# Optimization experiments

Measured on AMD Instinct MI355X. Metric: run time of the kernel, lower is better.

## Reference

```python
import jax, jax.numpy as jnp
import numpy as np

TAU = 1.0      # gumbel-softmax temperature
ALPHA = 0.05   # mixprop alpha
GDEP = 1       # mixprop depth

B, C, H, W = 16, 512, 96, 96
N = 64  # n_classes / codebook size


def setup_inputs() -> dict:
    key = jax.random.key(0)
    ks = jax.random.split(key, 8)
    u = jax.random.uniform(ks[3], (B, N, H, W), dtype=jnp.float32, minval=1e-6, maxval=1.0 - 1e-6)
    gumbel_noise = -jnp.log(-jnp.log(u))  # standard Gumbel(0,1)
    return {
        "x": jax.random.normal(ks[0], (B, C, H, W), dtype=jnp.float32),
        "centers": jax.random.normal(ks[1], (N, C), dtype=jnp.float32) * 0.1,
        "A": jax.random.uniform(ks[2], (N, N), dtype=jnp.float32),
        "gumbel_noise": gumbel_noise,
        "W_bc": jax.random.normal(ks[4], (1, C), dtype=jnp.float32) * 0.05,
        "b_bc": jnp.zeros((1,), dtype=jnp.float32),
        "W_gcn": jax.random.normal(ks[5], (C, 2 * C), dtype=jnp.float32) * 0.03,
        "b_gcn": jnp.zeros((C,), dtype=jnp.float32),
    }


def _mixprop_centers(centers, A, W_gcn, b_gcn):
    # mixprop on the codebook: centers [N, C] viewed as x of shape [1, C, N, 1]
    n = A.shape[0]
    adj = A + jnp.eye(n, dtype=A.dtype)
    a = adj / adj.sum(axis=1, keepdims=True)           # row-normalized adjacency
    xg = centers.T[None, :, :, None]                    # [1, C, N, 1]
    h = xg
    outs = [h]
    for _ in range(GDEP):
        h = ALPHA * xg + (1.0 - ALPHA) * jnp.einsum('ncwl,vw->ncvl', h, a)
        outs.append(h)
    ho = jnp.concatenate(outs, axis=1)                  # [1, (GDEP+1)*C, N, 1]
    new_c = jnp.einsum('oc,bcvl->bovl', W_gcn, ho) + b_gcn[None, :, None, None]
    return new_c[0, :, :, 0].T                          # [N, C]


def reference(x, centers, A, gumbel_noise, W_bc, b_bc, W_gcn, b_gcn):
    n = centers.shape[0]
    # inner products of features with codebook centers
    inner_products = jnp.einsum('bchw,nc->bnhw', x, centers)          # [B, N, H, W]
    # gumbel-softmax with hard (straight-through) assignment over dim 1
    y = jax.nn.softmax((inner_products + gumbel_noise) / TAU, axis=1)
    hard = jax.nn.one_hot(jnp.argmax(y, axis=1), n, dtype=y.dtype, axis=1)
    one_hot = hard + y - jax.lax.stop_gradient(y)
    # quantized features via codebook gather
    z_q = jnp.einsum('bnhw,nd->bdhw', one_hot, centers)               # [B, C, H, W]
    # 1x1 conv binary classifier + global average pool
    heatmap = jnp.einsum('oc,bchw->bohw', W_bc, z_q) + b_bc[None, :, None, None]  # [B,1,H,W]
    logits = heatmap.mean(axis=(2, 3)).squeeze()                      # [B]
    # graph diffusion of the codebook
    new_centers = _mixprop_centers(centers, A, W_gcn, b_gcn)          # [N, C]
    normed_ip = jnp.einsum('bchw,nc->bnhw', x, new_centers)           # [B, N, H, W]
    cluster_probs = jax.nn.one_hot(jnp.argmax(normed_ip, axis=1), n, dtype=normed_ip.dtype, axis=1)
    cluster_loss = -(cluster_probs * jax.nn.softmax(normed_ip, axis=1)).sum(axis=1).mean()
    return heatmap, logits, cluster_loss, inner_products
```

## Files before the change

kernel.cpp:

```cpp
#include <hip/hip_runtime.h>
#include <math.h>

#define BATCH   16
#define CDIM    512
#define HWDIM   9216
#define NCLS    64
#define TILE    128
#define NTILES  72
#define NCHUNK  16
#define NBLOCKS (NTILES * BATCH)

#define LOGOFF  147456
#define LOSSOFF 147472
#define IPOFF   147473

#define WS_S    65536
#define WS_PH   65600
#define WS_PC   66752
#define WS_AP   67904

typedef __attribute__((ext_vector_type(8))) short bf16x8;
typedef __attribute__((ext_vector_type(4))) float f32x4;

__device__ __forceinline__ void split3(float v, float& h, float& m, float& l) {
  float hf = __uint_as_float(__float_as_uint(v) & 0xFFFF0000u);
  float r  = v - hf;
  float mf = __uint_as_float(__float_as_uint(r) & 0xFFFF0000u);
  float r2 = r - mf;
  float lf = __uint_as_float(__float_as_uint(r2) & 0xFFFF0000u);
  h = hf; m = mf; l = lf;
}

__device__ __forceinline__ unsigned packbf(float a, float b) {
  return (__float_as_uint(a) >> 16) | (__float_as_uint(b) & 0xFFFF0000u);
}

__global__ __launch_bounds__(256) void prep_kernel(
    const float* __restrict__ centers, const float* __restrict__ Aadj,
    const float* __restrict__ W_bc, const float* __restrict__ b_bc,
    const float* __restrict__ W_gcn, const float* __restrict__ b_gcn,
    float* __restrict__ ws) {
  __shared__ float c_row[CDIM];
  __shared__ float mix_row[CDIM];
  __shared__ float new_row[CDIM];
  __shared__ float a_n[NCLS];
  __shared__ float red[256];
  const int n = blockIdx.x;
  const int tid = threadIdx.x;

  if (tid < NCLS) a_n[tid] = Aadj[n * NCLS + tid] + (tid == n ? 1.0f : 0.0f);
  __syncthreads();
  if (tid == 0) {
    float ssum = 0.f;
    for (int w = 0; w < NCLS; ++w) ssum += a_n[w];
    red[0] = 1.0f / ssum;
  }
  __syncthreads();
  float inv = red[0];
  __syncthreads();
  if (tid < NCLS) a_n[tid] *= inv;
  __syncthreads();

  float p = 0.f;
  for (int c = tid; c < CDIM; c += 256) {
    float v = centers[n * CDIM + c];
    c_row[c] = v;
    float acc = 0.f;
    #pragma unroll 8
    for (int w = 0; w < NCLS; ++w) acc = fmaf(a_n[w], centers[w * CDIM + c], acc);
    mix_row[c] = 0.05f * v + 0.95f * acc;
    p = fmaf(W_bc[c], v, p);
  }
  red[tid] = p;
  __syncthreads();
  for (int st = 128; st > 0; st >>= 1) {
    if (tid < st) red[tid] += red[tid + st];
    __syncthreads();
  }
  if (tid == 0) ws[WS_S + n] = red[0] + b_bc[0];
  __syncthreads();

  for (int o = tid; o < CDIM; o += 256) {
    const float4* wr0 = (const float4*)(W_gcn + (size_t)o * 1024);
    const float4* wr1 = (const float4*)(W_gcn + (size_t)o * 1024 + 512);
    const float4* cr4 = (const float4*)c_row;
    const float4* mr4 = (const float4*)mix_row;
    float a0 = b_gcn[o], a1 = 0.f, a2 = 0.f, a3 = 0.f;
    #pragma unroll 4
    for (int qk = 0; qk < 128; ++qk) {
      float4 wv = wr0[qk], cv = cr4[qk];
      a0 = fmaf(wv.x, cv.x, a0);
      a1 = fmaf(wv.y, cv.y, a1);
      a2 = fmaf(wv.z, cv.z, a2);
      a3 = fmaf(wv.w, cv.w, a3);
    }
    #pragma unroll 4
    for (int qk = 0; qk < 128; ++qk) {
      float4 wv = wr1[qk], mv = mr4[qk];
      a0 = fmaf(wv.x, mv.x, a0);
      a1 = fmaf(wv.y, mv.y, a1);
      a2 = fmaf(wv.z, mv.z, a2);
      a3 = fmaf(wv.w, mv.w, a3);
    }
    new_row[o] = (a0 + a1) + (a2 + a3);
  }
  __syncthreads();

  if (tid < 128) {
    const int rowsel = tid >> 6;
    const int u = tid & 63;
    const int c = u >> 2, q = u & 3;
    const float* rbuf = rowsel ? new_row : c_row;
    const int mb = (rowsel ? 4 : 0) + (n >> 4);
    const int lane = q * 16 + (n & 15);
    float e[8];
    #pragma unroll
    for (int i = 0; i < 8; ++i) e[i] = rbuf[c * 32 + q * 8 + i];
    unsigned dh[4], dm[4], dl[4];
    #pragma unroll
    for (int d = 0; d < 4; ++d) {
      float h0, m0, l0, h1, m1, l1;
      split3(e[2 * d], h0, m0, l0);
      split3(e[2 * d + 1], h1, m1, l1);
      dh[d] = packbf(h0, h1); dm[d] = packbf(m0, m1); dl[d] = packbf(l0, l1);
    }
    float* dst = ws + WS_AP + (size_t)c * 6144 + (size_t)mb * 256 + (size_t)lane * 4;
    *(uint4*)(dst)        = make_uint4(dh[0], dh[1], dh[2], dh[3]);
    *(uint4*)(dst + 2048) = make_uint4(dm[0], dm[1], dm[2], dm[3]);
    *(uint4*)(dst + 4096) = make_uint4(dl[0], dl[1], dl[2], dl[3]);
  }
}

__global__ __launch_bounds__(256, 3) void main_kernel(
    const float* __restrict__ x, const float* __restrict__ gumbel,
    float* __restrict__ ws, float* __restrict__ out) {
  __shared__ char ldsmem[49152];
  __shared__ float s_sh[NCLS];
  char* buf0 = ldsmem;
  char* buf1 = ldsmem + 24576;

  const int tid = threadIdx.x;
  const int w = tid >> 6, l = tid & 63;
  const int tile = blockIdx.x, b = blockIdx.y;
  const int hw0 = tile * TILE;

  if (tid < NCLS) s_sh[tid] = ws[WS_S + tid];

  const float* xb = x + (size_t)b * CDIM * HWDIM;
  const float* pB = xb + (size_t)(w * 8) * HWDIM + hw0 + l;
  const char* ap = (const char*)(ws + WS_AP);
  const int la16 = l * 16;

  f32x4 cip[8], cnp[8];
  #pragma unroll
  for (int i = 0; i < 8; ++i) {
    cip[i] = (f32x4){0.f, 0.f, 0.f, 0.f};
    cnp[i] = (f32x4){0.f, 0.f, 0.f, 0.f};
  }

  float bre[16];
  bf16x8 A0[5], A1[5];

#define LOAD_A(AS, c_) do {                                                   \
    const char* asrc = ap + (size_t)(c_) * 24576;                             \
    AS[0] = *(const bf16x8*)(asrc + w * 1024 + la16);                         \
    AS[1] = *(const bf16x8*)(asrc + 8192 + w * 1024 + la16);                  \
    AS[2] = *(const bf16x8*)(asrc + 16384 + w * 1024 + la16);                 \
    AS[3] = *(const bf16x8*)(asrc + (4 + w) * 1024 + la16);                   \
    AS[4] = *(const bf16x8*)(asrc + 8192 + (4 + w) * 1024 + la16);            \
  } while (0)

#define LOAD_B(c_) do {                                                       \
    const size_t koff = (size_t)(c_) * 32 * HWDIM;                            \
    _Pragma("unroll")                                                         \
    for (int j = 0; j < 8; ++j) {                                             \
      bre[j]     = pB[koff + (size_t)j * HWDIM];                              \
      bre[8 + j] = pB[koff + (size_t)j * HWDIM + 64];                         \
    }                                                                         \
  } while (0)

#define WRITE_B(WB) do {                                                      \
    _Pragma("unroll")                                                         \
    for (int hh = 0; hh < 2; ++hh) {                                          \
      unsigned dh[4], dm[4], dl[4];                                           \
      _Pragma("unroll")                                                       \
      for (int d = 0; d < 4; ++d) {                                           \
        float h0, m0, l0, h1, m1, l1;                                         \
        split3(bre[hh * 8 + 2 * d], h0, m0, l0);                              \
        split3(bre[hh * 8 + 2 * d + 1], h1, m1, l1);                          \
        dh[d] = packbf(h0, h1); dm[d] = packbf(m0, m1); dl[d] = packbf(l0, l1);\
      }                                                                       \
      char* basep = (WB) + ((((l >> 4) + hh * 4) * 64) + (w << 4) + (l & 15)) * 16; \
      *(uint4*)(basep)         = make_uint4(dh[0], dh[1], dh[2], dh[3]);      \
      *(uint4*)(basep + 8192)  = make_uint4(dm[0], dm[1], dm[2], dm[3]);      \
      *(uint4*)(basep + 16384) = make_uint4(dl[0], dl[1], dl[2], dl[3]);      \
    }                                                                         \
  } while (0)

#define CHUNK(c_, RB, WB, AC, AN) do {                                        \
    if ((c_) + 1 < NCHUNK) { LOAD_A(AN, (c_) + 1); LOAD_B((c_) + 1); }        \
    _Pragma("unroll")                                                         \
    for (int nb = 0; nb < 8; ++nb) {                                          \
      bf16x8 bH = *(const bf16x8*)((RB) + nb * 1024 + la16);                  \
      bf16x8 bM = *(const bf16x8*)((RB) + 8192 + nb * 1024 + la16);           \
      bf16x8 bL = *(const bf16x8*)((RB) + 16384 + nb * 1024 + la16);          \
      cip[nb] = __builtin_amdgcn_mfma_f32_16x16x32_bf16(AC[0], bH, cip[nb], 0, 0, 0); \
      cip[nb] = __builtin_amdgcn_mfma_f32_16x16x32_bf16(AC[0], bM, cip[nb], 0, 0, 0); \
      cip[nb] = __builtin_amdgcn_mfma_f32_16x16x32_bf16(AC[1], bH, cip[nb], 0, 0, 0); \
      cip[nb] = __builtin_amdgcn_mfma_f32_16x16x32_bf16(AC[0], bL, cip[nb], 0, 0, 0); \
      cip[nb] = __builtin_amdgcn_mfma_f32_16x16x32_bf16(AC[1], bM, cip[nb], 0, 0, 0); \
      cip[nb] = __builtin_amdgcn_mfma_f32_16x16x32_bf16(AC[2], bH, cip[nb], 0, 0, 0); \
      cnp[nb] = __builtin_amdgcn_mfma_f32_16x16x32_bf16(AC[3], bH, cnp[nb], 0, 0, 0); \
      cnp[nb] = __builtin_amdgcn_mfma_f32_16x16x32_bf16(AC[3], bM, cnp[nb], 0, 0, 0); \
      cnp[nb] = __builtin_amdgcn_mfma_f32_16x16x32_bf16(AC[4], bH, cnp[nb], 0, 0, 0); \
    }                                                                         \
    if ((c_) + 1 < NCHUNK) WRITE_B(WB);                                       \
    __syncthreads();                                                          \
  } while (0)

  LOAD_A(A0, 0);
  LOAD_B(0);
  WRITE_B(buf0);
  __syncthreads();

  #pragma unroll 1
  for (int cc = 0; cc < NCHUNK; cc += 2) {
    CHUNK(cc, buf0, buf1, A0, A1);
    CHUNK(cc + 1, buf1, buf0, A1, A0);
  }

  float* pvv  = (float*)ldsmem;
  int*   pvi  = (int*)(ldsmem + 2048);
  float* pnm  = (float*)(ldsmem + 4096);
  float* pns  = (float*)(ldsmem + 6144);
  float* m2   = (float*)(ldsmem + 8192);
  float* hbuf = (float*)(ldsmem + 8704);
  float* cbuf = (float*)(ldsmem + 9216);

  const size_t bn = (size_t)b * NCLS;
  float* ipo = out + IPOFF;
  const int rbase = 16 * w + ((l >> 4) & 3) * 4;
  const int c15 = l & 15;

  float bv[8]; int bi[8]; float nm[8];
  #pragma unroll
  for (int nb = 0; nb < 8; ++nb) {
    const int hw = hw0 + nb * 16 + c15;
    float best = -1e30f; int besti = 0;
    #pragma unroll
    for (int r = 0; r < 4; ++r) {
      const int n = rbase + r;
      const float v = cip[nb][r];
      ipo[(bn + n) * HWDIM + hw] = v;
      const float t = v + gumbel[(bn + n) * HWDIM + hw];
      if (t > best) { best = t; besti = n; }
    }
    bv[nb] = best; bi[nb] = besti;
    float m = cnp[nb][0];
    m = fmaxf(m, cnp[nb][1]); m = fmaxf(m, cnp[nb][2]); m = fmaxf(m, cnp[nb][3]);
    nm[nb] = m;
  }
  #pragma unroll
  for (int nb = 0; nb < 8; ++nb) {
    #pragma unroll
    for (int mk = 16; mk <= 32; mk <<= 1) {
      float ov = __shfl_xor(bv[nb], mk);
      int   oi = __shfl_xor(bi[nb], mk);
      if (ov > bv[nb] || (ov == bv[nb] && oi < bi[nb])) { bv[nb] = ov; bi[nb] = oi; }
      nm[nb] = fmaxf(nm[nb], __shfl_xor(nm[nb], mk));
    }
  }
  if ((l >> 4) == 0) {
    #pragma unroll
    for (int nb = 0; nb < 8; ++nb) {
      pvv[w * 128 + nb * 16 + l] = bv[nb];
      pvi[w * 128 + nb * 16 + l] = bi[nb];
      pnm[w * 128 + nb * 16 + l] = nm[nb];
    }
  }
  __syncthreads();

  if (tid < 128) {
    float v = pvv[tid]; int i = pvi[tid];
    #pragma unroll
    for (int ww = 1; ww < 4; ++ww) {
      float v2 = pvv[ww * 128 + tid]; int i2 = pvi[ww * 128 + tid];
      if (v2 > v || (v2 == v && i2 < i)) { v = v2; i = i2; }
    }
    float h = s_sh[i];
    hbuf[tid] = h;
    out[(size_t)b * HWDIM + hw0 + tid] = h;
    float m = pnm[tid];
    #pragma unroll
    for (int ww = 1; ww < 4; ++ww) m = fmaxf(m, pnm[ww * 128 + tid]);
    m2[tid] = m;
  }
  __syncthreads();

  #pragma unroll
  for (int nb = 0; nb < 8; ++nb) {
    const float mm = m2[nb * 16 + c15];
    float s = __expf(cnp[nb][0] - mm) + __expf(cnp[nb][1] - mm)
            + __expf(cnp[nb][2] - mm) + __expf(cnp[nb][3] - mm);
    s += __shfl_xor(s, 16);
    s += __shfl_xor(s, 32);
    if ((l >> 4) == 0) pns[w * 128 + nb * 16 + l] = s;
  }
  __syncthreads();

  if (tid < 128) {
    float S = pns[tid] + pns[128 + tid] + pns[256 + tid] + pns[384 + tid];
    cbuf[tid] = 1.0f / S;
  }
  __syncthreads();

  if (tid < 64) {
    float hs = hbuf[tid] + hbuf[tid + 64];
    float cs = cbuf[tid] + cbuf[tid + 64];
    #pragma unroll
    for (int o = 32; o > 0; o >>= 1) {
      hs += __shfl_down(hs, o);
      cs += __shfl_down(cs, o);
    }
    if (tid == 0) {
      ws[WS_PH + b * NTILES + tile] = hs;
      ws[WS_PC + b * NTILES + tile] = cs;
    }
  }
#undef LOAD_A
#undef LOAD_B
#undef WRITE_B
#undef CHUNK
}

__global__ __launch_bounds__(256) void finish_kernel(
    const float* __restrict__ ws, float* __restrict__ out) {
  __shared__ double sred[256];
  const int tid = threadIdx.x;
  {
    int bb = tid >> 4, lane = tid & 15;
    double s = 0.0;
    for (int t = lane; t < NTILES; t += 16) s += (double)ws[WS_PH + bb * NTILES + t];
    #pragma unroll
    for (int o = 8; o > 0; o >>= 1) s += __shfl_down(s, o, 16);
    if (lane == 0) out[LOGOFF + bb] = (float)(s / (double)HWDIM);
  }
  double c = 0.0;
  for (int i = tid; i < BATCH * NTILES; i += 256) c += (double)ws[WS_PC + i];
  sred[tid] = c;
  __syncthreads();
  for (int st = 128; st > 0; st >>= 1) {
    if (tid < st) sred[tid] += sred[tid + st];
    __syncthreads();
  }
  if (tid == 0) out[LOSSOFF] = (float)(-sred[0] / (double)(BATCH * HWDIM));
}

extern "C" void kernel_launch(void* const* d_in, const int* in_sizes, int n_in,
                              void* d_out, int out_size, void* d_ws, size_t ws_size,
                              hipStream_t stream) {
  const float* x       = (const float*)d_in[0];
  const float* centers = (const float*)d_in[1];
  const float* Aadj    = (const float*)d_in[2];
  const float* gumbel  = (const float*)d_in[3];
  const float* W_bc    = (const float*)d_in[4];
  const float* b_bc    = (const float*)d_in[5];
  const float* W_gcn   = (const float*)d_in[6];
  const float* b_gcn   = (const float*)d_in[7];
  float* out = (float*)d_out;
  float* ws  = (float*)d_ws;

  hipLaunchKernelGGL(prep_kernel, dim3(NCLS), dim3(256), 0, stream,
                     centers, Aadj, W_bc, b_bc, W_gcn, b_gcn, ws);
  hipLaunchKernelGGL(main_kernel, dim3(NTILES, BATCH), dim3(256), 0, stream,
                     x, gumbel, ws, out);
  hipLaunchKernelGGL(finish_kernel, dim3(1), dim3(256), 0, stream, ws, out);
}
```

Before: 176.2 us.

## Switch main GEMM to 32x32x16 MFMA with 2x2 wave tiling

Replaces the 16x16x32 bf16 MFMA tiling (each wave owning 16 classes across 8 column blocks) with 32x32x16 MFMA, where waves form a 2x2 grid of 32-class by 64-column tiles. The prep kernel and the LDS B-staging layouts are rearranged to match the new operand fragment layout. The epilogue reductions are rewritten for the 32x32 accumulator layout, needing fewer cross-wave partials. This aims to cut LDS B-fragment reads per MFMA and use the larger MFMA shape, at the cost of doubling the A-fragment registers held per wave.

```diff
diff --git a/kernel.cpp b/kernel.cpp
--- a/kernel.cpp
+++ b/kernel.cpp
@@ -8,7 +8,6 @@
 #define TILE    128
 #define NTILES  72
 #define NCHUNK  16
-#define NBLOCKS (NTILES * BATCH)
 
 #define LOGOFF  147456
 #define LOSSOFF 147472
@@ -20,7 +19,7 @@
 #define WS_AP   67904
 
 typedef __attribute__((ext_vector_type(8))) short bf16x8;
-typedef __attribute__((ext_vector_type(4))) float f32x4;
+typedef __attribute__((ext_vector_type(16))) float f32x16;
 
 __device__ __forceinline__ void split3(float v, float& h, float& m, float& l) {
   float hf = __uint_as_float(__float_as_uint(v) & 0xFFFF0000u);
@@ -109,13 +108,15 @@
   if (tid < 128) {
     const int rowsel = tid >> 6;
     const int u = tid & 63;
-    const int c = u >> 2, q = u & 3;
+    const int c = u >> 2;
+    const int s = (u >> 1) & 1;
+    const int hh = u & 1;
     const float* rbuf = rowsel ? new_row : c_row;
-    const int mb = (rowsel ? 4 : 0) + (n >> 4);
-    const int lane = q * 16 + (n & 15);
+    const int mt = (rowsel ? 2 : 0) + (n >> 5);
+    const int lane = (n & 31) + 32 * hh;
     float e[8];
     #pragma unroll
-    for (int i = 0; i < 8; ++i) e[i] = rbuf[c * 32 + q * 8 + i];
+    for (int i = 0; i < 8; ++i) e[i] = rbuf[c * 32 + s * 16 + hh * 8 + i];
     unsigned dh[4], dm[4], dl[4];
     #pragma unroll
     for (int d = 0; d < 4; ++d) {
@@ -124,7 +125,7 @@
       split3(e[2 * d + 1], h1, m1, l1);
       dh[d] = packbf(h0, h1); dm[d] = packbf(m0, m1); dl[d] = packbf(l0, l1);
     }
-    float* dst = ws + WS_AP + (size_t)c * 6144 + (size_t)mb * 256 + (size_t)lane * 4;
+    float* dst = ws + WS_AP + (size_t)c * 6144 + (size_t)(s * 4 + mt) * 256 + (size_t)lane * 4;
     *(uint4*)(dst)        = make_uint4(dh[0], dh[1], dh[2], dh[3]);
     *(uint4*)(dst + 2048) = make_uint4(dm[0], dm[1], dm[2], dm[3]);
     *(uint4*)(dst + 4096) = make_uint4(dl[0], dl[1], dl[2], dl[3]);
@@ -141,79 +142,94 @@
 
   const int tid = threadIdx.x;
   const int w = tid >> 6, l = tid & 63;
+  const int mh = w & 1, nh = w >> 1;
+  const int h = l >> 5, c31 = l & 31;
   const int tile = blockIdx.x, b = blockIdx.y;
   const int hw0 = tile * TILE;
 
   if (tid < NCLS) s_sh[tid] = ws[WS_S + tid];
 
   const float* xb = x + (size_t)b * CDIM * HWDIM;
-  const float* pB = xb + (size_t)(w * 8) * HWDIM + hw0 + l;
+  const float* pB = xb + (size_t)(h * 8) * HWDIM + hw0 + w * 32 + c31;
   const char* ap = (const char*)(ws + WS_AP);
   const int la16 = l * 16;
 
-  f32x4 cip[8], cnp[8];
+  f32x16 cip[2], cnp[2];
   #pragma unroll
-  for (int i = 0; i < 8; ++i) {
-    cip[i] = (f32x4){0.f, 0.f, 0.f, 0.f};
-    cnp[i] = (f32x4){0.f, 0.f, 0.f, 0.f};
+  for (int i = 0; i < 2; ++i) {
+    cip[i] = (f32x16)(0.f);
+    cnp[i] = (f32x16)(0.f);
   }
 
   float bre[16];
-  bf16x8 A0[5], A1[5];
+  bf16x8 A0[10], A1[10];
 
 #define LOAD_A(AS, c_) do {                                                   \
     const char* asrc = ap + (size_t)(c_) * 24576;                             \
-    AS[0] = *(const bf16x8*)(asrc + w * 1024 + la16);                         \
-    AS[1] = *(const bf16x8*)(asrc + 8192 + w * 1024 + la16);                  \
-    AS[2] = *(const bf16x8*)(asrc + 16384 + w * 1024 + la16);                 \
-    AS[3] = *(const bf16x8*)(asrc + (4 + w) * 1024 + la16);                   \
-    AS[4] = *(const bf16x8*)(asrc + 8192 + (4 + w) * 1024 + la16);            \
+    AS[0] = *(const bf16x8*)(asrc + (0 + mh) * 1024 + la16);                  \
+    AS[1] = *(const bf16x8*)(asrc + 8192 + (0 + mh) * 1024 + la16);           \
+    AS[2] = *(const bf16x8*)(asrc + 16384 + (0 + mh) * 1024 + la16);          \
+    AS[3] = *(const bf16x8*)(asrc + (2 + mh) * 1024 + la16);                  \
+    AS[4] = *(const bf16x8*)(asrc + 8192 + (2 + mh) * 1024 + la16);           \
+    AS[5] = *(const bf16x8*)(asrc + (4 + mh) * 1024 + la16);                  \
+    AS[6] = *(const bf16x8*)(asrc + 8192 + (4 + mh) * 1024 + la16);          \
+    AS[7] = *(const bf16x8*)(asrc + 16384 + (4 + mh) * 1024 + la16);         \
+    AS[8] = *(const bf16x8*)(asrc + (6 + mh) * 1024 + la16);                  \
+    AS[9] = *(const bf16x8*)(asrc + 8192 + (6 + mh) * 1024 + la16);          \
   } while (0)
 
 #define LOAD_B(c_) do {                                                       \
     const size_t koff = (size_t)(c_) * 32 * HWDIM;                            \
     _Pragma("unroll")                                                         \
-    for (int j = 0; j < 8; ++j) {                                             \
-      bre[j]     = pB[koff + (size_t)j * HWDIM];                              \
-      bre[8 + j] = pB[koff + (size_t)j * HWDIM + 64];                         \
+    for (int e = 0; e < 8; ++e) {                                             \
+      bre[e]     = pB[koff + (size_t)e * HWDIM];                              \
+      bre[8 + e] = pB[koff + (size_t)(16 + e) * HWDIM];                       \
     }                                                                         \
   } while (0)
 
 #define WRITE_B(WB) do {                                                      \
     _Pragma("unroll")                                                         \
-    for (int hh = 0; hh < 2; ++hh) {                                          \
+    for (int s = 0; s < 2; ++s) {                                             \
       unsigned dh[4], dm[4], dl[4];                                           \
       _Pragma("unroll")                                                       \
       for (int d = 0; d < 4; ++d) {                                           \
         float h0, m0, l0, h1, m1, l1;                                         \
-        split3(bre[hh * 8 + 2 * d], h0, m0, l0);                              \
-        split3(bre[hh * 8 + 2 * d + 1], h1, m1, l1);                          \
+        split3(bre[s * 8 + 2 * d], h0, m0, l0);                               \
+        split3(bre[s * 8 + 2 * d + 1], h1, m1, l1);                           \
         dh[d] = packbf(h0, h1); dm[d] = packbf(m0, m1); dl[d] = packbf(l0, l1);\
       }                                                                       \
-      char* basep = (WB) + ((((l >> 4) + hh * 4) * 64) + (w << 4) + (l & 15)) * 16; \
+      char* basep = (WB) + (s * 4 + w) * 1024 + la16;                         \
       *(uint4*)(basep)         = make_uint4(dh[0], dh[1], dh[2], dh[3]);      \
       *(uint4*)(basep + 8192)  = make_uint4(dm[0], dm[1], dm[2], dm[3]);      \
       *(uint4*)(basep + 16384) = make_uint4(dl[0], dl[1], dl[2], dl[3]);      \
     }                                                                         \
   } while (0)
 
+#define MFMA32 __builtin_amdgcn_mfma_f32_32x32x16_bf16
+
+#define PHASE_S(RB, AC, S, OFF) do {                                          \
+    _Pragma("unroll")                                                         \
+    for (int nt = 0; nt < 2; ++nt) {                                          \
+      const int nn = nh * 2 + nt;                                             \
+      bf16x8 bH = *(const bf16x8*)((RB) + ((S) * 4 + nn) * 1024 + la16);      \
+      bf16x8 bM = *(const bf16x8*)((RB) + 8192 + ((S) * 4 + nn) * 1024 + la16); \
+      bf16x8 bL = *(const bf16x8*)((RB) + 16384 + ((S) * 4 + nn) * 1024 + la16); \
+      cip[nt] = MFMA32(AC[OFF + 0], bH, cip[nt], 0, 0, 0);                    \
+      cip[nt] = MFMA32(AC[OFF + 0], bM, cip[nt], 0, 0, 0);                    \
+      cip[nt] = MFMA32(AC[OFF + 1], bH, cip[nt], 0, 0, 0);                    \
+      cip[nt] = MFMA32(AC[OFF + 0], bL, cip[nt], 0, 0, 0);                    \
+      cip[nt] = MFMA32(AC[OFF + 1], bM, cip[nt], 0, 0, 0);                    \
+      cip[nt] = MFMA32(AC[OFF + 2], bH, cip[nt], 0, 0, 0);                    \
+      cnp[nt] = MFMA32(AC[OFF + 3], bH, cnp[nt], 0, 0, 0);                    \
+      cnp[nt] = MFMA32(AC[OFF + 3], bM, cnp[nt], 0, 0, 0);                    \
+      cnp[nt] = MFMA32(AC[OFF + 4], bH, cnp[nt], 0, 0, 0);                    \
+    }                                                                         \
+  } while (0)
+
 #define CHUNK(c_, RB, WB, AC, AN) do {                                        \
     if ((c_) + 1 < NCHUNK) { LOAD_A(AN, (c_) + 1); LOAD_B((c_) + 1); }        \
-    _Pragma("unroll")                                                         \
-    for (int nb = 0; nb < 8; ++nb) {                                          \
-      bf16x8 bH = *(const bf16x8*)((RB) + nb * 1024 + la16);                  \
-      bf16x8 bM = *(const bf16x8*)((RB) + 8192 + nb * 1024 + la16);           \
-      bf16x8 bL = *(const bf16x8*)((RB) + 16384 + nb * 1024 + la16);          \
-      cip[nb] = __builtin_amdgcn_mfma_f32_16x16x32_bf16(AC[0], bH, cip[nb], 0, 0, 0); \
-      cip[nb] = __builtin_amdgcn_mfma_f32_16x16x32_bf16(AC[0], bM, cip[nb], 0, 0, 0); \
-      cip[nb] = __builtin_amdgcn_mfma_f32_16x16x32_bf16(AC[1], bH, cip[nb], 0, 0, 0); \
-      cip[nb] = __builtin_amdgcn_mfma_f32_16x16x32_bf16(AC[0], bL, cip[nb], 0, 0, 0); \
-      cip[nb] = __builtin_amdgcn_mfma_f32_16x16x32_bf16(AC[1], bM, cip[nb], 0, 0, 0); \
-      cip[nb] = __builtin_amdgcn_mfma_f32_16x16x32_bf16(AC[2], bH, cip[nb], 0, 0, 0); \
-      cnp[nb] = __builtin_amdgcn_mfma_f32_16x16x32_bf16(AC[3], bH, cnp[nb], 0, 0, 0); \
-      cnp[nb] = __builtin_amdgcn_mfma_f32_16x16x32_bf16(AC[3], bM, cnp[nb], 0, 0, 0); \
-      cnp[nb] = __builtin_amdgcn_mfma_f32_16x16x32_bf16(AC[4], bH, cnp[nb], 0, 0, 0); \
-    }                                                                         \
+    PHASE_S(RB, AC, 0, 0);                                                    \
+    PHASE_S(RB, AC, 1, 5);                                                    \
     if ((c_) + 1 < NCHUNK) WRITE_B(WB);                                       \
     __syncthreads();                                                          \
   } while (0)
@@ -230,86 +246,72 @@
   }
 
   float* pvv  = (float*)ldsmem;
-  int*   pvi  = (int*)(ldsmem + 2048);
-  float* pnm  = (float*)(ldsmem + 4096);
-  float* pns  = (float*)(ldsmem + 6144);
-  float* m2   = (float*)(ldsmem + 8192);
-  float* hbuf = (float*)(ldsmem + 8704);
-  float* cbuf = (float*)(ldsmem + 9216);
+  int*   pvi  = (int*)(ldsmem + 1024);
+  float* pnm  = (float*)(ldsmem + 2048);
+  float* pns  = (float*)(ldsmem + 3072);
+  float* m2   = (float*)(ldsmem + 4096);
+  float* hbuf = (float*)(ldsmem + 4608);
+  float* cbuf = (float*)(ldsmem + 5120);
 
   const size_t bn = (size_t)b * NCLS;
   float* ipo = out + IPOFF;
-  const int rbase = 16 * w + ((l >> 4) & 3) * 4;
-  const int c15 = l & 15;
-
-  float bv[8]; int bi[8]; float nm[8];
+
   #pragma unroll
-  for (int nb = 0; nb < 8; ++nb) {
-    const int hw = hw0 + nb * 16 + c15;
-    float best = -1e30f; int besti = 0;
-    #pragma unroll
-    for (int r = 0; r < 4; ++r) {
-      const int n = rbase + r;
-      const float v = cip[nb][r];
-      ipo[(bn + n) * HWDIM + hw] = v;
-      const float t = v + gumbel[(bn + n) * HWDIM + hw];
-      if (t > best) { best = t; besti = n; }
-    }
-    bv[nb] = best; bi[nb] = besti;
-    float m = cnp[nb][0];
-    m = fmaxf(m, cnp[nb][1]); m = fmaxf(m, cnp[nb][2]); m = fmaxf(m, cnp[nb][3]);
-    nm[nb] = m;
-  }
-  #pragma unroll
-  for (int nb = 0; nb < 8; ++nb) {
-    #pragma unroll
-    for (int mk = 16; mk <= 32; mk <<= 1) {
-      float ov = __shfl_xor(bv[nb], mk);
-      int   oi = __shfl_xor(bi[nb], mk);
-      if (ov > bv[nb] || (ov == bv[nb] && oi < bi[nb])) { bv[nb] = ov; bi[nb] = oi; }
-      nm[nb] = fmaxf(nm[nb], __shfl_xor(nm[nb], mk));
-    }
-  }
-  if ((l >> 4) == 0) {
-    #pragma unroll
-    for (int nb = 0; nb < 8; ++nb) {
-      pvv[w * 128 + nb * 16 + l] = bv[nb];
-      pvi[w * 128 + nb * 16 + l] = bi[nb];
-      pnm[w * 128 + nb * 16 + l] = nm[nb];
+  for (int nt = 0; nt < 2; ++nt) {
+    const int col = nh * 64 + nt * 32 + c31;
+    const int gcol = hw0 + col;
+    float best = -1e30f; int bi = 0;
+    #pragma unroll
+    for (int r = 0; r < 16; ++r) {
+      const int nrow = mh * 32 + (r & 3) + 8 * (r >> 2) + 4 * h;
+      const size_t off = (bn + nrow) * HWDIM + gcol;
+      const float v = cip[nt][r];
+      ipo[off] = v;
+      const float t = v + gumbel[off];
+      if (t > best) { best = t; bi = nrow; }
+    }
+    {
+      float ov = __shfl_xor(best, 32);
+      int   oi = __shfl_xor(bi, 32);
+      if (ov > best || (ov == best && oi < bi)) { best = ov; bi = oi; }
+    }
+    float mx = -1e30f;
+    #pragma unroll
+    for (int r = 0; r < 16; ++r) mx = fmaxf(mx, cnp[nt][r]);
+    mx = fmaxf(mx, __shfl_xor(mx, 32));
+    if (h == 0) {
+      pvv[mh * 128 + col] = best;
+      pvi[mh * 128 + col] = bi;
+      pnm[mh * 128 + col] = mx;
     }
   }
   __syncthreads();
 
   if (tid < 128) {
     float v = pvv[tid]; int i = pvi[tid];
-    #pragma unroll
-    for (int ww = 1; ww < 4; ++ww) {
-      float v2 = pvv[ww * 128 + tid]; int i2 = pvi[ww * 128 + tid];
-      if (v2 > v || (v2 == v && i2 < i)) { v = v2; i = i2; }
-    }
-    float h = s_sh[i];
-    hbuf[tid] = h;
-    out[(size_t)b * HWDIM + hw0 + tid] = h;
-    float m = pnm[tid];
-    #pragma unroll
-    for (int ww = 1; ww < 4; ++ww) m = fmaxf(m, pnm[ww * 128 + tid]);
-    m2[tid] = m;
+    float v2 = pvv[128 + tid]; int i2 = pvi[128 + tid];
+    if (v2 > v || (v2 == v && i2 < i)) { v = v2; i = i2; }
+    float hh2 = s_sh[i];
+    hbuf[tid] = hh2;
+    out[(size_t)b * HWDIM + hw0 + tid] = hh2;
+    m2[tid] = fmaxf(pnm[tid], pnm[128 + tid]);
   }
   __syncthreads();
 
   #pragma unroll
-  for (int nb = 0; nb < 8; ++nb) {
-    const float mm = m2[nb * 16 + c15];
-    float s = __expf(cnp[nb][0] - mm) + __expf(cnp[nb][1] - mm)
-            + __expf(cnp[nb][2] - mm) + __expf(cnp[nb][3] - mm);
-    s += __shfl_xor(s, 16);
-    s += __shfl_xor(s, 32);
-    if ((l >> 4) == 0) pns[w * 128 + nb * 16 + l] = s;
+  for (int nt = 0; nt < 2; ++nt) {
+    const int col = nh * 64 + nt * 32 + c31;
+    const float mm = m2[col];
+    float se = 0.f;
+    #pragma unroll
+    for (int r = 0; r < 16; ++r) se += __expf(cnp[nt][r] - mm);
+    se += __shfl_xor(se, 32);
+    if (h == 0) pns[mh * 128 + col] = se;
   }
   __syncthreads();
 
   if (tid < 128) {
-    float S = pns[tid] + pns[128 + tid] + pns[256 + tid] + pns[384 + tid];
+    float S = pns[tid] + pns[128 + tid];
     cbuf[tid] = 1.0f / S;
   }
   __syncthreads();
@@ -330,7 +332,9 @@
 #undef LOAD_A
 #undef LOAD_B
 #undef WRITE_B
+#undef PHASE_S
 #undef CHUNK
+#undef MFMA32
 }
 
 __global__ __launch_bounds__(256) void finish_kernel(
```

New measurement: 243.8 us. 1.38x slower.
